# Kernel optimization log

Hardware: AMD Instinct MI355X
Metric: run time of the kernel (lower is better)

Reference implementation:

```python
import jax, jax.numpy as jnp
import numpy as np

N = 50000      # nodes
E = 1_600_000  # edges
IN, H, H2, OUT = 256, 128, 64, 2
EPS = 1e-5     # BatchNorm eps


def setup_inputs() -> dict:
    key = jax.random.key(0)
    ks = jax.random.split(key, 18)
    inp = {
        "x": jax.random.normal(ks[0], (N, IN), dtype=jnp.float32),
        "edge_index": jax.random.randint(ks[1], (2, E), 0, N, dtype=jnp.int64),
        # GCNConv 1
        "W1": jax.random.normal(ks[2], (IN, H), dtype=jnp.float32) / np.sqrt(IN),
        "b1": jnp.zeros((H,), dtype=jnp.float32),
        "g1": jnp.ones((H,), dtype=jnp.float32),
        "be1": jnp.zeros((H,), dtype=jnp.float32),
        "m1": jax.random.normal(ks[3], (H,), dtype=jnp.float32) * 0.1,
        "v1": jax.random.uniform(ks[4], (H,), dtype=jnp.float32, minval=0.5, maxval=1.5),
        # GCNConv 2
        "W2": jax.random.normal(ks[5], (H, H2), dtype=jnp.float32) / np.sqrt(H),
        "b2": jnp.zeros((H2,), dtype=jnp.float32),
        "g2": jnp.ones((H2,), dtype=jnp.float32),
        "be2": jnp.zeros((H2,), dtype=jnp.float32),
        "m2": jax.random.normal(ks[6], (H2,), dtype=jnp.float32) * 0.1,
        "v2": jax.random.uniform(ks[7], (H2,), dtype=jnp.float32, minval=0.5, maxval=1.5),
        # final linear
        "Wl": jax.random.normal(ks[8], (H2, OUT), dtype=jnp.float32) / np.sqrt(H2),
        "bl": jnp.zeros((OUT,), dtype=jnp.float32),
    }
    return inp


def _gcn_conv(x, W, b, src, dst, n_nodes):
    # PyG GCNConv: linear transform, then symmetric-normalized aggregation
    # with self-loops (gcn_norm, improved=False, fill_value=1).
    xw = x @ W                                            # [N, H]
    ones = jnp.ones((src.shape[0],), dtype=x.dtype)
    deg = jax.ops.segment_sum(ones, dst, num_segments=n_nodes) + 1.0  # +1 self-loop
    dinv = jax.lax.rsqrt(deg)                             # deg^{-1/2}
    norm = dinv[src] * dinv[dst]                          # [E]
    msgs = xw[src] * norm[:, None]                        # [E, H] gather
    agg = jax.ops.segment_sum(msgs, dst, num_segments=n_nodes)  # scatter-add
    agg = agg + xw * (1.0 / deg)[:, None]                 # self-loop term
    return agg + b


def _bn_relu(x, gamma, beta, mean, var):
    # inference-mode BatchNorm1d + ReLU
    xhat = (x - mean) * jax.lax.rsqrt(var + EPS)
    return jax.nn.relu(xhat * gamma + beta)


def reference(x, edge_index, W1, b1, g1, be1, m1, v1,
              W2, b2, g2, be2, m2, v2, Wl, bl):
    src, dst = edge_index[0], edge_index[1]
    h = _gcn_conv(x, W1, b1, src, dst, N)
    h = _bn_relu(h, g1, be1, m1, v1)
    # dropout is identity in eval mode
    h = _gcn_conv(h, W2, b2, src, dst, N)
    h = _bn_relu(h, g2, be2, m2, v2)
    return h @ Wl + bl
```

## Files before the change

### kernel.cpp

```cpp
#include <hip/hip_runtime.h>

#define N_NODES 50000
#define N_EDGES 1600000
#define IN_F 256
#define H1_F 128
#define H2_F 64
#define OUT_F 2
#define BN_EPS 1e-5f

#define NBUK 782
#define BCAP 3584
#define CHUNK 2048
#define NCHUNK 782

typedef __attribute__((ext_vector_type(8))) short bf16x8;
typedef __attribute__((ext_vector_type(4))) float f32x4;
typedef __attribute__((ext_vector_type(4))) int   i32x4;
typedef __attribute__((ext_vector_type(4))) unsigned u32x4;

__device__ __forceinline__ unsigned short f2b(float f) {
    union { float f; unsigned u; } v; v.f = f;
    unsigned r = (v.u + 0x7FFFu + ((v.u >> 16) & 1u)) >> 16;
    return (unsigned short)r;
}
__device__ __forceinline__ float b2f(unsigned short b) {
    union { unsigned u; float f; } v; v.u = ((unsigned)b) << 16;
    return v.f;
}
__device__ __forceinline__ void add2(float& a0, float& a1, unsigned u) {
    union { unsigned u; float f; } lo, hi;
    lo.u = u << 16;
    hi.u = u & 0xFFFF0000u;
    a0 += lo.f; a1 += hi.f;
}

__launch_bounds__(256)
__global__ void chist_kernel(const int* __restrict__ dst, int* __restrict__ h,
                             int* __restrict__ tot) {
    __shared__ int lh[NBUK];
    const int c = blockIdx.x;
    for (int i = threadIdx.x; i < NBUK; i += 256) lh[i] = 0;
    __syncthreads();
    const int e0 = c * CHUNK;
    const int e1 = min(e0 + CHUNK, N_EDGES);
    const i32x4* p = (const i32x4*)(dst + e0);
    const int n4 = (e1 - e0) >> 2;
    for (int i = threadIdx.x; i < n4; i += 256) {
        i32x4 d = __builtin_nontemporal_load(p + i);
        atomicAdd(&lh[d.x >> 6], 1);
        atomicAdd(&lh[d.y >> 6], 1);
        atomicAdd(&lh[d.z >> 6], 1);
        atomicAdd(&lh[d.w >> 6], 1);
    }
    __syncthreads();
    for (int i = threadIdx.x; i < NBUK; i += 256) {
        int v = lh[i];
        h[(size_t)i * NCHUNK + c] = v;
        if (v) atomicAdd(&tot[i], v);
    }
}

__global__ void bscan_kernel(const int* __restrict__ tot, int* __restrict__ boff,
                             int* __restrict__ rowptr) {
    __shared__ int tmp[1024];
    const int t = threadIdx.x;
    int v = (t < NBUK) ? tot[t] : 0;
    tmp[t] = v;
    __syncthreads();
    for (int off = 1; off < 1024; off <<= 1) {
        int a = (t >= off) ? tmp[t - off] : 0;
        __syncthreads();
        tmp[t] += a;
        __syncthreads();
    }
    if (t < NBUK) boff[t] = tmp[t] - v;
    if (t == 0) { boff[NBUK] = N_EDGES; rowptr[N_NODES] = N_EDGES; }
}

__launch_bounds__(256)
__global__ void boffs_kernel(int* __restrict__ h, const int* __restrict__ boff) {
    const int b = (blockIdx.x * blockDim.x + threadIdx.x) >> 6;
    if (b >= NBUK) return;
    const int lane = threadIdx.x & 63;
    int run = boff[b];
    int* row = h + (size_t)b * NCHUNK;
    for (int c0 = 0; c0 < NCHUNK; c0 += 64) {
        int idx = c0 + lane;
        int v = (idx < NCHUNK) ? row[idx] : 0;
        int s = v;
#pragma unroll
        for (int off = 1; off < 64; off <<= 1) {
            int t = __shfl_up(s, off);
            if (lane >= off) s += t;
        }
        if (idx < NCHUNK) row[idx] = run + (s - v);
        run += __shfl(s, 63);
    }
}

__launch_bounds__(256)
__global__ void cscatter_kernel(const int* __restrict__ src, const int* __restrict__ dst,
                                const int* __restrict__ h, unsigned* __restrict__ bedges) {
    __shared__ int cur[NBUK];
    const int c = blockIdx.x;
    for (int i = threadIdx.x; i < NBUK; i += 256) cur[i] = h[(size_t)i * NCHUNK + c];
    __syncthreads();
    const int e0 = c * CHUNK;
    const int e1 = min(e0 + CHUNK, N_EDGES);
    const i32x4* pd = (const i32x4*)(dst + e0);
    const i32x4* ps = (const i32x4*)(src + e0);
    const int n4 = (e1 - e0) >> 2;
    for (int i = threadIdx.x; i < n4; i += 256) {
        i32x4 d = __builtin_nontemporal_load(pd + i);
        i32x4 s = __builtin_nontemporal_load(ps + i);
        int slot;
        slot = atomicAdd(&cur[d.x >> 6], 1); bedges[slot] = (unsigned)s.x | ((unsigned)d.x << 16);
        slot = atomicAdd(&cur[d.y >> 6], 1); bedges[slot] = (unsigned)s.y | ((unsigned)d.y << 16);
        slot = atomicAdd(&cur[d.z >> 6], 1); bedges[slot] = (unsigned)s.z | ((unsigned)d.z << 16);
        slot = atomicAdd(&cur[d.w >> 6], 1); bedges[slot] = (unsigned)s.w | ((unsigned)d.w << 16);
    }
}

__launch_bounds__(256)
__global__ void build_kernel(const unsigned* __restrict__ bedges, const int* __restrict__ boff,
                             unsigned short* __restrict__ perm, int* __restrict__ rowptr,
                             float* __restrict__ dinv) {
    __shared__ unsigned e_lds[BCAP];
    __shared__ unsigned short p_lds[BCAP];
    __shared__ int ncnt[64], ncur[64];

    const int b = blockIdx.x;
    const int t = threadIdx.x;
    const int start = boff[b];
    const int end   = boff[b + 1];
    const int cnt   = end - start;
    const bool fits = (cnt <= BCAP);

    if (t < 64) ncnt[t] = 0;
    __syncthreads();

    for (int i = t; i < cnt; i += 256) {
        unsigned e = bedges[start + i];
        if (fits) e_lds[i] = e;
        atomicAdd(&ncnt[(e >> 16) & 63], 1);
    }
    __syncthreads();

    if (t == 0) {
        int a = 0;
        for (int i = 0; i < 64; ++i) { ncur[i] = a; a += ncnt[i]; }
    }
    __syncthreads();

    if (t < 64) {
        int node = b * 64 + t;
        if (node < N_NODES) {
            rowptr[node] = start + ncur[t];
            dinv[node]   = rsqrtf((float)ncnt[t] + 1.0f);
        }
    }
    __syncthreads();

    for (int i = t; i < cnt; i += 256) {
        unsigned e = fits ? e_lds[i] : bedges[start + i];
        int slot = atomicAdd(&ncur[(e >> 16) & 63], 1);
        unsigned short s = (unsigned short)(e & 0xFFFFu);
        if (fits) p_lds[slot] = s;
        else      perm[start + slot] = s;
    }
    if (fits) {
        __syncthreads();
        for (int i = t; i < cnt; i += 256) perm[start + i] = p_lds[i];
    }
}

__global__ void wt_kernel(const float* __restrict__ W, unsigned short* __restrict__ WT,
                          int K, int N) {
    int i = blockIdx.x * blockDim.x + threadIdx.x;
    if (i < N * K) {
        int n = i / K, k = i % K;
        WT[i] = f2b(W[(size_t)k * N + n]);
    }
}

__global__ void bnprep_kernel(const float* __restrict__ g, const float* __restrict__ be,
                              const float* __restrict__ m, const float* __restrict__ v,
                              const float* __restrict__ bias, float* __restrict__ sc,
                              float* __restrict__ sh, int F) {
    int f = blockIdx.x * blockDim.x + threadIdx.x;
    if (f < F) {
        float s = g[f] * rsqrtf(v[f] + BN_EPS);
        sc[f] = s;
        sh[f] = (bias[f] - m[f]) * s + be[f];
    }
}

template <int KSTEPS, int NTILES, bool A_BF16>
__launch_bounds__(256)
__global__ void mfma_gemm_kernel(const void* __restrict__ Ap, const unsigned short* __restrict__ BT,
                                 const float* __restrict__ dscale, unsigned short* __restrict__ C,
                                 int M) {
    constexpr int K  = KSTEPS * 32;
    constexpr int NF = NTILES * 16;
    const int wave = threadIdx.x >> 6;
    const int lane = threadIdx.x & 63;
    const int r0   = (blockIdx.x * 4 + wave) * 16;
    const int m    = lane & 15;
    const int kb   = lane >> 4;

    int arow = r0 + m;
    if (arow >= M) arow = M - 1;

    f32x4 acc[NTILES];
#pragma unroll
    for (int nt = 0; nt < NTILES; ++nt) acc[nt] = (f32x4)(0.f);

#pragma unroll
    for (int ks = 0; ks < KSTEPS; ++ks) {
        const int k0 = ks * 32 + kb * 8;
        bf16x8 a;
        if constexpr (A_BF16) {
            a = *(const bf16x8*)((const unsigned short*)Ap + (size_t)arow * K + k0);
        } else {
            const float* af = (const float*)Ap + (size_t)arow * K + k0;
            f32x4 lo = __builtin_nontemporal_load((const f32x4*)af);
            f32x4 hi = __builtin_nontemporal_load((const f32x4*)(af + 4));
            union { bf16x8 v; unsigned short u[8]; } pk;
            pk.u[0] = f2b(lo.x); pk.u[1] = f2b(lo.y); pk.u[2] = f2b(lo.z); pk.u[3] = f2b(lo.w);
            pk.u[4] = f2b(hi.x); pk.u[5] = f2b(hi.y); pk.u[6] = f2b(hi.z); pk.u[7] = f2b(hi.w);
            a = pk.v;
        }
#pragma unroll
        for (int nt = 0; nt < NTILES; ++nt) {
            bf16x8 b = *(const bf16x8*)(BT + (size_t)(nt * 16 + m) * K + k0);
            acc[nt] = __builtin_amdgcn_mfma_f32_16x16x32_bf16(a, b, acc[nt], 0, 0, 0);
        }
    }

#pragma unroll
    for (int reg = 0; reg < 4; ++reg) {
        const int r = r0 + kb * 4 + reg;
        if (r < M) {
            const float ds = dscale[r];
#pragma unroll
            for (int nt = 0; nt < NTILES; ++nt)
                C[(size_t)r * NF + nt * 16 + m] = f2b(acc[nt][reg] * ds);
        }
    }
}

template <int HF, bool FINAL>
__launch_bounds__(256)
__global__ void agg_kernel(const int* __restrict__ rowptr, const unsigned short* __restrict__ perm,
                           const unsigned short* __restrict__ xw, const float* __restrict__ dinv,
                           const float* __restrict__ sc, const float* __restrict__ sh,
                           const float* __restrict__ Wl, const float* __restrict__ bl,
                           void* __restrict__ outp) {
    constexpr int LPE = HF / 8;
    constexpr int G   = 64 / LPE;
    const int wave = threadIdx.x >> 6;
    const int node = blockIdx.x * 4 + wave;
    if (node >= N_NODES) return;
    const int lane = threadIdx.x & 63;
    const int grp  = lane / LPE;
    const int fl   = (lane % LPE) * 8;

    float aA[8];
#pragma unroll
    for (int i = 0; i < 8; ++i) aA[i] = 0.f;

    if (grp == 0) {
        u32x4 u = *(const u32x4*)(xw + (size_t)node * HF + fl);
#pragma unroll
        for (int i = 0; i < 4; ++i) add2(aA[2 * i], aA[2 * i + 1], u[i]);
    }

    const int start = rowptr[node];
    const int end   = rowptr[node + 1];
    for (int base = start; base < end; base += 64) {
        int pidx = base + lane;
        int pv = (int)__builtin_nontemporal_load(perm + (pidx < end ? pidx : end - 1));
        int ne = end - base;
        if (ne > 64) ne = 64;
        if (ne == 64) {
#pragma unroll
            for (int j = 0; j < 64; j += G) {
                int s = __shfl(pv, j + grp);
                u32x4 u = *(const u32x4*)(xw + (size_t)s * HF + fl);
#pragma unroll
                for (int i = 0; i < 4; ++i) add2(aA[2 * i], aA[2 * i + 1], u[i]);
            }
        } else {
            for (int j = 0; j < ne; j += G) {
                int s = __shfl(pv, j + grp);
                if (j + grp < ne) {
                    u32x4 u = *(const u32x4*)(xw + (size_t)s * HF + fl);
#pragma unroll
                    for (int i = 0; i < 4; ++i) add2(aA[2 * i], aA[2 * i + 1], u[i]);
                }
            }
        }
    }

#pragma unroll
    for (int off = LPE; off < 64; off <<= 1)
#pragma unroll
        for (int i = 0; i < 8; ++i) aA[i] += __shfl_xor(aA[i], off);

    const float dv = dinv[node];
    f32x4 scl = *(const f32x4*)(sc + fl);
    f32x4 sch = *(const f32x4*)(sc + fl + 4);
    f32x4 shl = *(const f32x4*)(sh + fl);
    f32x4 shh = *(const f32x4*)(sh + fl + 4);
    float y[8];
#pragma unroll
    for (int i = 0; i < 4; ++i) {
        y[i]     = fmaxf(aA[i] * (dv * scl[i]) + shl[i], 0.f);
        y[i + 4] = fmaxf(aA[i + 4] * (dv * sch[i]) + shh[i], 0.f);
    }

    if constexpr (!FINAL) {
        if (lane < LPE) {
            u32x4 o;
#pragma unroll
            for (int i = 0; i < 4; ++i)
                o[i] = (unsigned)f2b(y[2 * i]) | ((unsigned)f2b(y[2 * i + 1]) << 16);
            __builtin_nontemporal_store(o, (u32x4*)((unsigned short*)outp + (size_t)node * HF + fl));
        }
    } else {
        float p0 = 0.f, p1 = 0.f;
#pragma unroll
        for (int i = 0; i < 8; ++i) {
            p0 += y[i] * Wl[(fl + i) * 2 + 0];
            p1 += y[i] * Wl[(fl + i) * 2 + 1];
        }
#pragma unroll
        for (int off = 1; off < LPE; off <<= 1) {
            p0 += __shfl_xor(p0, off);
            p1 += __shfl_xor(p1, off);
        }
        if (lane == 0) {
            float* o = (float*)outp;
            o[(size_t)node * 2 + 0] = p0 + bl[0];
            o[(size_t)node * 2 + 1] = p1 + bl[1];
        }
    }
}

extern "C" void kernel_launch(void* const* d_in, const int* in_sizes, int n_in,
                              void* d_out, int out_size, void* d_ws, size_t ws_size,
                              hipStream_t stream) {
    const float* x   = (const float*)d_in[0];
    const int*   ei  = (const int*)d_in[1];
    const float* W1  = (const float*)d_in[2];
    const float* b1  = (const float*)d_in[3];
    const float* g1  = (const float*)d_in[4];
    const float* be1 = (const float*)d_in[5];
    const float* m1  = (const float*)d_in[6];
    const float* v1  = (const float*)d_in[7];
    const float* W2  = (const float*)d_in[8];
    const float* b2  = (const float*)d_in[9];
    const float* g2  = (const float*)d_in[10];
    const float* be2 = (const float*)d_in[11];
    const float* m2  = (const float*)d_in[12];
    const float* v2  = (const float*)d_in[13];
    const float* Wl  = (const float*)d_in[14];
    const float* bl  = (const float*)d_in[15];

    const int* src = ei;
    const int* dst = ei + N_EDGES;

    int*            h      = (int*)d_ws;
    int*            tot    = h + (size_t)NBUK * NCHUNK;
    int*            boff   = tot + 1024;
    int*            rowptr = boff + 1024;
    float*          dinv   = (float*)(rowptr + 50016);
    float*          sc1    = dinv + 50016;
    float*          sh1    = sc1 + 128;
    float*          sc2    = sh1 + 128;
    float*          sh2    = sc2 + 64;
    unsigned*       bedges = (unsigned*)(sh2 + 64);
    unsigned short* perm   = (unsigned short*)(bedges + N_EDGES);
    unsigned short* xwb    = perm + N_EDGES;
    unsigned short* h1b    = xwb + (size_t)N_NODES * H1_F;
    unsigned short* w1t    = h1b + (size_t)N_NODES * H1_F;
    unsigned short* w2t    = w1t + H1_F * IN_F;

    hipMemsetAsync(tot, 0, 1024 * sizeof(int), stream);

    chist_kernel<<<NCHUNK, 256, 0, stream>>>(dst, h, tot);
    bscan_kernel<<<1, 1024, 0, stream>>>(tot, boff, rowptr);
    boffs_kernel<<<(NBUK * 64 + 255) / 256, 256, 0, stream>>>(h, boff);
    cscatter_kernel<<<NCHUNK, 256, 0, stream>>>(src, dst, h, bedges);
    build_kernel<<<NBUK, 256, 0, stream>>>(bedges, boff, perm, rowptr, dinv);

    wt_kernel<<<(H1_F * IN_F + 255) / 256, 256, 0, stream>>>(W1, w1t, IN_F, H1_F);
    wt_kernel<<<(H2_F * H1_F + 255) / 256, 256, 0, stream>>>(W2, w2t, H1_F, H2_F);
    bnprep_kernel<<<1, 128, 0, stream>>>(g1, be1, m1, v1, b1, sc1, sh1, H1_F);
    bnprep_kernel<<<1, 64, 0, stream>>>(g2, be2, m2, v2, b2, sc2, sh2, H2_F);

    mfma_gemm_kernel<IN_F / 32, H1_F / 16, false><<<(N_NODES + 63) / 64, 256, 0, stream>>>(
        x, w1t, dinv, xwb, N_NODES);
    agg_kernel<H1_F, false><<<(N_NODES + 3) / 4, 256, 0, stream>>>(
        rowptr, perm, xwb, dinv, sc1, sh1, nullptr, nullptr, h1b);

    mfma_gemm_kernel<H1_F / 32, H2_F / 16, true><<<(N_NODES + 63) / 64, 256, 0, stream>>>(
        h1b, w2t, dinv, xwb, N_NODES);
    agg_kernel<H2_F, true><<<(N_NODES + 3) / 4, 256, 0, stream>>>(
        rowptr, perm, xwb, dinv, sc2, sh2, Wl, bl, (float*)d_out);
}
```

Before: 270.3 us.

## Process eight nodes per wave in aggregation, merge prep kernels, enlarge edge chunks

Measured after the change: 299.7 us. +10.9%, slower.

```diff
diff --git a/kernel.cpp b/kernel.cpp
--- a/kernel.cpp
+++ b/kernel.cpp
@@ -10,8 +10,9 @@
 
 #define NBUK 782
 #define BCAP 3584
-#define CHUNK 2048
-#define NCHUNK 782
+#define CHUNK 4096
+#define NCHUNK 391
+#define NPW 8
 
 typedef __attribute__((ext_vector_type(8))) short bf16x8;
 typedef __attribute__((ext_vector_type(4))) float f32x4;
@@ -174,24 +175,37 @@
     }
 }
 
-__global__ void wt_kernel(const float* __restrict__ W, unsigned short* __restrict__ WT,
-                          int K, int N) {
-    int i = blockIdx.x * blockDim.x + threadIdx.x;
-    if (i < N * K) {
-        int n = i / K, k = i % K;
-        WT[i] = f2b(W[(size_t)k * N + n]);
-    }
-}
-
-__global__ void bnprep_kernel(const float* __restrict__ g, const float* __restrict__ be,
-                              const float* __restrict__ m, const float* __restrict__ v,
-                              const float* __restrict__ bias, float* __restrict__ sc,
-                              float* __restrict__ sh, int F) {
-    int f = blockIdx.x * blockDim.x + threadIdx.x;
-    if (f < F) {
-        float s = g[f] * rsqrtf(v[f] + BN_EPS);
-        sc[f] = s;
-        sh[f] = (bias[f] - m[f]) * s + be[f];
+__global__ void prep_kernel(const float* __restrict__ W1, const float* __restrict__ W2,
+                            unsigned short* __restrict__ w1t, unsigned short* __restrict__ w2t,
+                            const float* __restrict__ g1, const float* __restrict__ be1,
+                            const float* __restrict__ m1, const float* __restrict__ v1,
+                            const float* __restrict__ b1,
+                            const float* __restrict__ g2, const float* __restrict__ be2,
+                            const float* __restrict__ m2, const float* __restrict__ v2,
+                            const float* __restrict__ b2,
+                            float* __restrict__ sc1, float* __restrict__ sh1,
+                            float* __restrict__ sc2, float* __restrict__ sh2) {
+    const int blk = blockIdx.x;
+    const int t = threadIdx.x;
+    if (blk < 128) {
+        int i = blk * 256 + t;
+        int n = i / IN_F, k = i % IN_F;
+        w1t[i] = f2b(W1[(size_t)k * H1_F + n]);
+    } else if (blk < 160) {
+        int i = (blk - 128) * 256 + t;
+        int n = i / H1_F, k = i % H1_F;
+        w2t[i] = f2b(W2[(size_t)k * H2_F + n]);
+    } else {
+        if (t < H1_F) {
+            float s = g1[t] * rsqrtf(v1[t] + BN_EPS);
+            sc1[t] = s;
+            sh1[t] = (b1[t] - m1[t]) * s + be1[t];
+        } else if (t < H1_F + H2_F) {
+            int f = t - H1_F;
+            float s = g2[f] * rsqrtf(v2[f] + BN_EPS);
+            sc2[f] = s;
+            sh2[f] = (b2[f] - m2[f]) * s + be2[f];
+        }
     }
 }
 
@@ -258,91 +272,108 @@
                            void* __restrict__ outp) {
     constexpr int LPE = HF / 8;
     constexpr int G   = 64 / LPE;
-    const int wave = threadIdx.x >> 6;
-    const int node = blockIdx.x * 4 + wave;
-    if (node >= N_NODES) return;
+    const int wid  = (blockIdx.x * blockDim.x + threadIdx.x) >> 6;
+    const int n0   = wid * NPW;
+    if (n0 >= N_NODES) return;
     const int lane = threadIdx.x & 63;
     const int grp  = lane / LPE;
     const int fl   = (lane % LPE) * 8;
 
-    float aA[8];
-#pragma unroll
-    for (int i = 0; i < 8; ++i) aA[i] = 0.f;
-
-    if (grp == 0) {
-        u32x4 u = *(const u32x4*)(xw + (size_t)node * HF + fl);
-#pragma unroll
-        for (int i = 0; i < 4; ++i) add2(aA[2 * i], aA[2 * i + 1], u[i]);
-    }
-
-    const int start = rowptr[node];
-    const int end   = rowptr[node + 1];
-    for (int base = start; base < end; base += 64) {
-        int pidx = base + lane;
-        int pv = (int)__builtin_nontemporal_load(perm + (pidx < end ? pidx : end - 1));
-        int ne = end - base;
-        if (ne > 64) ne = 64;
-        if (ne == 64) {
-#pragma unroll
-            for (int j = 0; j < 64; j += G) {
-                int s = __shfl(pv, j + grp);
-                u32x4 u = *(const u32x4*)(xw + (size_t)s * HF + fl);
-#pragma unroll
-                for (int i = 0; i < 4; ++i) add2(aA[2 * i], aA[2 * i + 1], u[i]);
-            }
-        } else {
-            for (int j = 0; j < ne; j += G) {
-                int s = __shfl(pv, j + grp);
-                if (j + grp < ne) {
-                    u32x4 u = *(const u32x4*)(xw + (size_t)s * HF + fl);
-#pragma unroll
-                    for (int i = 0; i < 4; ++i) add2(aA[2 * i], aA[2 * i + 1], u[i]);
-                }
-            }
-        }
-    }
-
-#pragma unroll
-    for (int off = LPE; off < 64; off <<= 1)
-#pragma unroll
-        for (int i = 0; i < 8; ++i) aA[i] += __shfl_xor(aA[i], off);
-
-    const float dv = dinv[node];
     f32x4 scl = *(const f32x4*)(sc + fl);
     f32x4 sch = *(const f32x4*)(sc + fl + 4);
     f32x4 shl = *(const f32x4*)(sh + fl);
     f32x4 shh = *(const f32x4*)(sh + fl + 4);
-    float y[8];
-#pragma unroll
-    for (int i = 0; i < 4; ++i) {
-        y[i]     = fmaxf(aA[i] * (dv * scl[i]) + shl[i], 0.f);
-        y[i + 4] = fmaxf(aA[i + 4] * (dv * sch[i]) + shh[i], 0.f);
-    }
-
-    if constexpr (!FINAL) {
-        if (lane < LPE) {
-            u32x4 o;
-#pragma unroll
-            for (int i = 0; i < 4; ++i)
-                o[i] = (unsigned)f2b(y[2 * i]) | ((unsigned)f2b(y[2 * i + 1]) << 16);
-            __builtin_nontemporal_store(o, (u32x4*)((unsigned short*)outp + (size_t)node * HF + fl));
-        }
-    } else {
-        float p0 = 0.f, p1 = 0.f;
+    float wl0[8], wl1[8];
+    if constexpr (FINAL) {
 #pragma unroll
         for (int i = 0; i < 8; ++i) {
-            p0 += y[i] * Wl[(fl + i) * 2 + 0];
-            p1 += y[i] * Wl[(fl + i) * 2 + 1];
-        }
-#pragma unroll
-        for (int off = 1; off < LPE; off <<= 1) {
-            p0 += __shfl_xor(p0, off);
-            p1 += __shfl_xor(p1, off);
-        }
-        if (lane == 0) {
-            float* o = (float*)outp;
-            o[(size_t)node * 2 + 0] = p0 + bl[0];
-            o[(size_t)node * 2 + 1] = p1 + bl[1];
+            wl0[i] = Wl[(fl + i) * 2 + 0];
+            wl1[i] = Wl[(fl + i) * 2 + 1];
+        }
+    }
+
+    int rp = 0;
+    if (lane <= NPW) rp = rowptr[n0 + lane];
+    float dvl = (lane < NPW) ? dinv[n0 + lane] : 0.f;
+
+    for (int k = 0; k < NPW; ++k) {
+        const int node  = n0 + k;
+        const int start = __shfl(rp, k);
+        const int end   = __shfl(rp, k + 1);
+
+        float aA[8];
+#pragma unroll
+        for (int i = 0; i < 8; ++i) aA[i] = 0.f;
+
+        if (grp == 0) {
+            u32x4 u = *(const u32x4*)(xw + (size_t)node * HF + fl);
+#pragma unroll
+            for (int i = 0; i < 4; ++i) add2(aA[2 * i], aA[2 * i + 1], u[i]);
+        }
+
+        for (int base = start; base < end; base += 64) {
+            int pidx = base + lane;
+            int pv = (int)__builtin_nontemporal_load(perm + (pidx < end ? pidx : end - 1));
+            int ne = end - base;
+            if (ne > 64) ne = 64;
+            if (ne == 64) {
+#pragma unroll
+                for (int j = 0; j < 64; j += G) {
+                    int s = __shfl(pv, j + grp);
+                    u32x4 u = *(const u32x4*)(xw + (size_t)s * HF + fl);
+#pragma unroll
+                    for (int i = 0; i < 4; ++i) add2(aA[2 * i], aA[2 * i + 1], u[i]);
+                }
+            } else {
+                for (int j = 0; j < ne; j += G) {
+                    int s = __shfl(pv, j + grp);
+                    if (j + grp < ne) {
+                        u32x4 u = *(const u32x4*)(xw + (size_t)s * HF + fl);
+#pragma unroll
+                        for (int i = 0; i < 4; ++i) add2(aA[2 * i], aA[2 * i + 1], u[i]);
+                    }
+                }
+            }
+        }
+
+#pragma unroll
+        for (int off = LPE; off < 64; off <<= 1)
+#pragma unroll
+            for (int i = 0; i < 8; ++i) aA[i] += __shfl_xor(aA[i], off);
+
+        const float dv = __shfl(dvl, k);
+        float y[8];
+#pragma unroll
+        for (int i = 0; i < 4; ++i) {
+            y[i]     = fmaxf(aA[i] * (dv * scl[i]) + shl[i], 0.f);
+            y[i + 4] = fmaxf(aA[i + 4] * (dv * sch[i]) + shh[i], 0.f);
+        }
+
+        if constexpr (!FINAL) {
+            if (lane < LPE) {
+                u32x4 o;
+#pragma unroll
+                for (int i = 0; i < 4; ++i)
+                    o[i] = (unsigned)f2b(y[2 * i]) | ((unsigned)f2b(y[2 * i + 1]) << 16);
+                __builtin_nontemporal_store(o, (u32x4*)((unsigned short*)outp + (size_t)node * HF + fl));
+            }
+        } else {
+            float p0 = 0.f, p1 = 0.f;
+#pragma unroll
+            for (int i = 0; i < 8; ++i) {
+                p0 += y[i] * wl0[i];
+                p1 += y[i] * wl1[i];
+            }
+#pragma unroll
+            for (int off = 1; off < LPE; off <<= 1) {
+                p0 += __shfl_xor(p0, off);
+                p1 += __shfl_xor(p1, off);
+            }
+            if (lane == 0) {
+                float* o = (float*)outp;
+                o[(size_t)node * 2 + 0] = p0 + bl[0];
+                o[(size_t)node * 2 + 1] = p1 + bl[1];
+            }
         }
     }
 }
@@ -394,18 +425,18 @@
     cscatter_kernel<<<NCHUNK, 256, 0, stream>>>(src, dst, h, bedges);
     build_kernel<<<NBUK, 256, 0, stream>>>(bedges, boff, perm, rowptr, dinv);
 
-    wt_kernel<<<(H1_F * IN_F + 255) / 256, 256, 0, stream>>>(W1, w1t, IN_F, H1_F);
-    wt_kernel<<<(H2_F * H1_F + 255) / 256, 256, 0, stream>>>(W2, w2t, H1_F, H2_F);
-    bnprep_kernel<<<1, 128, 0, stream>>>(g1, be1, m1, v1, b1, sc1, sh1, H1_F);
-    bnprep_kernel<<<1, 64, 0, stream>>>(g2, be2, m2, v2, b2, sc2, sh2, H2_F);
+    prep_kernel<<<161, 256, 0, stream>>>(W1, W2, w1t, w2t,
+                                         g1, be1, m1, v1, b1,
+                                         g2, be2, m2, v2, b2,
+                                         sc1, sh1, sc2, sh2);
 
     mfma_gemm_kernel<IN_F / 32, H1_F / 16, false><<<(N_NODES + 63) / 64, 256, 0, stream>>>(
         x, w1t, dinv, xwb, N_NODES);
-    agg_kernel<H1_F, false><<<(N_NODES + 3) / 4, 256, 0, stream>>>(
+    agg_kernel<H1_F, false><<<(N_NODES / NPW + 3) / 4, 256, 0, stream>>>(
         rowptr, perm, xwb, dinv, sc1, sh1, nullptr, nullptr, h1b);
 
     mfma_gemm_kernel<H1_F / 32, H2_F / 16, true><<<(N_NODES + 63) / 64, 256, 0, stream>>>(
         h1b, w2t, dinv, xwb, N_NODES);
-    agg_kernel<H2_F, true><<<(N_NODES + 3) / 4, 256, 0, stream>>>(
+    agg_kernel<H2_F, true><<<(N_NODES / NPW + 3) / 4, 256, 0, stream>>>(
         rowptr, perm, xwb, dinv, sc2, sh2, Wl, bl, (float*)d_out);
 }
```
